# Kernel tuning notes

Hardware: AMD Instinct MI355X
Metric: run time of the kernel (lower is better)

The kernel has to match this reference:

```python
import jax, jax.numpy as jnp
import numpy as np

LN_EPS = 1e-5


def _ln(x, g, b):
    m = x.mean(-1, keepdims=True)
    v = ((x - m) ** 2).mean(-1, keepdims=True)
    return (x - m) * jax.lax.rsqrt(v + LN_EPS) * g + b


def setup_inputs() -> dict:
    key = jax.random.key(0)
    ks = jax.random.split(key, 8)
    B, S, T, Ds, Dt, H = 2, 1024, 1024, 128, 64, 64

    def w(k, shp):
        return jax.random.normal(k, shp, dtype=jnp.float32) * 0.05

    return {
        "source_features": jax.random.normal(ks[0], (B, S, Ds), dtype=jnp.float32),
        "target_features": jax.random.normal(ks[1], (B, T, Dt), dtype=jnp.float32),
        # source_adapter: Linear(Ds,H) -> LN(H) -> ReLU -> Linear(H,H)
        "sW1": w(ks[2], (Ds, H)), "sb1": jnp.zeros(H), "sg": jnp.ones(H), "sbeta": jnp.zeros(H),
        "sW2": w(ks[3], (H, H)), "sb2": jnp.zeros(H),
        # target_adapter: Linear(Dt,H) -> LN(H) -> ReLU -> Linear(H,H)
        "tW1": w(ks[4], (Dt, H)), "tb1": jnp.zeros(H), "tg": jnp.ones(H), "tbeta": jnp.zeros(H),
        "tW2": w(ks[5], (H, H)), "tb2": jnp.zeros(H),
        # city_features: Linear(2H,H) -> LN(H) -> ReLU
        "cW": w(ks[6], (2 * H, H)), "cb": jnp.zeros(H), "cg": jnp.ones(H), "cbeta": jnp.zeros(H),
        # similarity_module: Linear(H,1) -> Sigmoid
        "simW": w(ks[7], (H, 1)), "simb": jnp.zeros(1),
    }


def reference(source_features, target_features,
              sW1, sb1, sg, sbeta, sW2, sb2,
              tW1, tb1, tg, tbeta, tW2, tb2,
              cW, cb, cg, cbeta, simW, simb):
    H = sW2.shape[1]
    s_ad = jax.nn.relu(_ln(source_features @ sW1 + sb1, sg, sbeta)) @ sW2 + sb2  # [B,S,H]
    t_ad = jax.nn.relu(_ln(target_features @ tW1 + tb1, tg, tbeta)) @ tW2 + tb2  # [B,T,H]

    # concat order in torch is [target, source] on the last dim; split the
    # Linear(2H,H) weight so the [B,T,S,2H] concat is never materialized.
    cW_t, cW_s = cW[:H], cW[H:]
    pre = (t_ad @ cW_t)[:, :, None, :] + (s_ad @ cW_s)[:, None, :, :] + cb  # [B,T,S,H]
    h = jax.nn.relu(_ln(pre, cg, cbeta))
    scores = jax.nn.sigmoid((h @ simW)[..., 0] + simb[0])  # [B,T,S]

    attn = jax.nn.softmax(scores, axis=-1)
    transferred = jnp.einsum('bts,bsh->bth', attn, s_ad)
    gate = jax.nn.sigmoid(t_ad.mean(-1, keepdims=True))
    adapted = t_ad * (1.0 - gate) + transferred * gate  # hidden_dim == target_dim: no proj
    return adapted, scores
```

## Files before the change

kernel.cpp:

```cpp
#include <hip/hip_runtime.h>
#include <math.h>

#define BN 2
#define SN 1024
#define TN 1024
#define DS 128
#define DT 64
#define HN 64
#define LN_EPS 1e-5f

typedef float v2f __attribute__((ext_vector_type(2)));

__device__ __forceinline__ float wave_sum(float v) {
#pragma unroll
  for (int m = 32; m >= 1; m >>= 1) v += __shfl_xor(v, m, 64);
  return v;
}

__device__ __forceinline__ v2f lo2(float4 v) { v2f r = {v.x, v.y}; return r; }
__device__ __forceinline__ v2f hi2(float4 v) { v2f r = {v.z, v.w}; return r; }

__global__ __launch_bounds__(256) void k_adapters(
    const float* __restrict__ src, const float* __restrict__ tgt,
    const float* __restrict__ sW1, const float* __restrict__ sb1,
    const float* __restrict__ sg, const float* __restrict__ sbeta,
    const float* __restrict__ sW2, const float* __restrict__ sb2,
    const float* __restrict__ tW1, const float* __restrict__ tb1,
    const float* __restrict__ tg, const float* __restrict__ tbeta,
    const float* __restrict__ tW2, const float* __restrict__ tb2,
    const float* __restrict__ cW, const float* __restrict__ cb,
    float* __restrict__ s_ad, float* __restrict__ sc, float* __restrict__ sstats,
    float* __restrict__ t_ad, float* __restrict__ tc, float* __restrict__ tstats)
{
  __shared__ float xbuf[4][DS];
  __shared__ float rbuf[4][HN];
  int w = threadIdx.x >> 6, lane = threadIdx.x & 63;

  if (blockIdx.x < 512) {
    int row = blockIdx.x * 4 + w;
    xbuf[w][lane]      = src[row * DS + lane];
    xbuf[w][lane + 64] = src[row * DS + 64 + lane];
    float a0 = 0.f, a1 = 0.f, a2_ = 0.f, a3 = 0.f;
#pragma unroll 8
    for (int k = 0; k < DS; k += 4) {
      a0  = fmaf(xbuf[w][k + 0], sW1[(k + 0) * HN + lane], a0);
      a1  = fmaf(xbuf[w][k + 1], sW1[(k + 1) * HN + lane], a1);
      a2_ = fmaf(xbuf[w][k + 2], sW1[(k + 2) * HN + lane], a2_);
      a3  = fmaf(xbuf[w][k + 3], sW1[(k + 3) * HN + lane], a3);
    }
    float h1 = ((a0 + a1) + (a2_ + a3)) + sb1[lane];
    float s1 = wave_sum(h1), s2 = wave_sum(h1 * h1);
    float m = s1 * (1.f / HN);
    float var = s2 * (1.f / HN) - m * m;
    float r = fmaxf(0.f, (h1 - m) * rsqrtf(var + LN_EPS) * sg[lane] + sbeta[lane]);
    rbuf[w][lane] = r;
    float b0 = 0.f, b1 = 0.f, b2 = 0.f, b3 = 0.f;
#pragma unroll 4
    for (int j = 0; j < HN; j += 4) {
      b0 = fmaf(rbuf[w][j + 0], sW2[(j + 0) * HN + lane], b0);
      b1 = fmaf(rbuf[w][j + 1], sW2[(j + 1) * HN + lane], b1);
      b2 = fmaf(rbuf[w][j + 2], sW2[(j + 2) * HN + lane], b2);
      b3 = fmaf(rbuf[w][j + 3], sW2[(j + 3) * HN + lane], b3);
    }
    float a2 = ((b0 + b1) + (b2 + b3)) + sb2[lane];
    s_ad[row * HN + lane] = a2;
    rbuf[w][lane] = a2;
    float c0 = 0.f, c1 = 0.f, c2 = 0.f, c3 = 0.f;
#pragma unroll 4
    for (int j = 0; j < HN; j += 4) {
      c0 = fmaf(rbuf[w][j + 0], cW[(HN + j + 0) * HN + lane], c0);
      c1 = fmaf(rbuf[w][j + 1], cW[(HN + j + 1) * HN + lane], c1);
      c2 = fmaf(rbuf[w][j + 2], cW[(HN + j + 2) * HN + lane], c2);
      c3 = fmaf(rbuf[w][j + 3], cW[(HN + j + 3) * HN + lane], c3);
    }
    float scv = (c0 + c1) + (c2 + c3);
    sc[row * HN + lane] = scv;
    float bs = wave_sum(scv), qs = wave_sum(scv * scv);
    if (lane == 0) { sstats[row * 2] = bs; sstats[row * 2 + 1] = qs; }
  } else {
    int row = (blockIdx.x - 512) * 4 + w;
    xbuf[w][lane] = tgt[row * DT + lane];
    float a0 = 0.f, a1 = 0.f, a2_ = 0.f, a3 = 0.f;
#pragma unroll 4
    for (int k = 0; k < DT; k += 4) {
      a0  = fmaf(xbuf[w][k + 0], tW1[(k + 0) * HN + lane], a0);
      a1  = fmaf(xbuf[w][k + 1], tW1[(k + 1) * HN + lane], a1);
      a2_ = fmaf(xbuf[w][k + 2], tW1[(k + 2) * HN + lane], a2_);
      a3  = fmaf(xbuf[w][k + 3], tW1[(k + 3) * HN + lane], a3);
    }
    float h1 = ((a0 + a1) + (a2_ + a3)) + tb1[lane];
    float s1 = wave_sum(h1), s2 = wave_sum(h1 * h1);
    float m = s1 * (1.f / HN);
    float var = s2 * (1.f / HN) - m * m;
    float r = fmaxf(0.f, (h1 - m) * rsqrtf(var + LN_EPS) * tg[lane] + tbeta[lane]);
    rbuf[w][lane] = r;
    float b0 = 0.f, b1 = 0.f, b2 = 0.f, b3 = 0.f;
#pragma unroll 4
    for (int j = 0; j < HN; j += 4) {
      b0 = fmaf(rbuf[w][j + 0], tW2[(j + 0) * HN + lane], b0);
      b1 = fmaf(rbuf[w][j + 1], tW2[(j + 1) * HN + lane], b1);
      b2 = fmaf(rbuf[w][j + 2], tW2[(j + 2) * HN + lane], b2);
      b3 = fmaf(rbuf[w][j + 3], tW2[(j + 3) * HN + lane], b3);
    }
    float a2 = ((b0 + b1) + (b2 + b3)) + tb2[lane];
    t_ad[row * HN + lane] = a2;
    float asum = wave_sum(a2);
    float gate = 1.f / (1.f + __expf(-asum * (1.f / HN)));
    rbuf[w][lane] = a2;
    float c0 = 0.f, c1 = 0.f, c2 = 0.f, c3 = 0.f;
#pragma unroll 4
    for (int j = 0; j < HN; j += 4) {
      c0 = fmaf(rbuf[w][j + 0], cW[(j + 0) * HN + lane], c0);
      c1 = fmaf(rbuf[w][j + 1], cW[(j + 1) * HN + lane], c1);
      c2 = fmaf(rbuf[w][j + 2], cW[(j + 2) * HN + lane], c2);
      c3 = fmaf(rbuf[w][j + 3], cW[(j + 3) * HN + lane], c3);
    }
    float tcv = ((c0 + c1) + (c2 + c3)) + cb[lane];
    tc[row * HN + lane] = tcv;
    float A = wave_sum(tcv), Q = wave_sum(tcv * tcv);
    if (lane == 0) { tstats[row * 3] = A; tstats[row * 3 + 1] = Q; tstats[row * 3 + 2] = gate; }
  }
}

#define ROWDW 68
#define CHUNKDW (64 * ROWDW)

__global__ __attribute__((amdgpu_flat_work_group_size(512, 512)))
__attribute__((amdgpu_waves_per_eu(4, 4)))
void k_scores(
    const float* __restrict__ cg, const float* __restrict__ cbeta,
    const float* __restrict__ simW, const float* __restrict__ simb,
    const float* __restrict__ sc, const float* __restrict__ sstats,
    const float* __restrict__ tc, const float* __restrict__ tstats,
    float* __restrict__ out_scores)
{
  __shared__ float tile[2 * CHUNKDW];
  int tid = threadIdx.x;
  int w = tid >> 6, lane = tid & 63;
  int sblk = blockIdx.x & 3;
  int tblk = (blockIdx.x >> 2) & 63;
  int b    = blockIdx.x >> 8;
  int t0 = tblk * 16 + w * 2;
  int rt0 = __builtin_amdgcn_readfirstlane(b * TN + t0);
  int rt1 = rt0 + 1;

  float A0  = tstats[rt0 * 3 + 0];
  float Qt0 = tstats[rt0 * 3 + 1];
  float A1  = tstats[rt1 * 3 + 0];
  float Qt1 = tstats[rt1 * 3 + 1];
  const float4* tq0 = (const float4*)(tc + rt0 * HN);
  const float4* tq1 = (const float4*)(tc + rt1 * HN);
  const float4* cgq = (const float4*)cg;
  const float4* cbq = (const float4*)cbeta;
  const float4* swq = (const float4*)simW;
  float simb0 = simb[0];

  const float4* scg = (const float4*)(sc + b * SN * HN);
  int s0 = sblk * 256;

  int r0s = tid >> 4, gs = tid & 15;
  int d0 = r0s * ROWDW + gs * 4;
  int d1 = d0 + 32 * ROWDW;

  {
    float4 v0 = scg[(s0 + r0s) * 16 + gs];
    float4 v1 = scg[(s0 + r0s + 32) * 16 + gs];
    *(float4*)&tile[d0] = v0;
    *(float4*)&tile[d1] = v1;
  }
  __syncthreads();

  const v2f zero2 = {0.f, 0.f};

#pragma unroll 1
  for (int c = 0; c < 4; ++c) {
    float4 p0, p1;
    if (c < 3) {
      int sn = s0 + (c + 1) * 64;
      p0 = scg[(sn + r0s) * 16 + gs];
      p1 = scg[(sn + r0s + 32) * 16 + gs];
    }

    const float* tb_ = &tile[(c & 1) * CHUNKDW + lane * ROWDW];
    int s = s0 + c * 64 + lane;
    float2 bq = *(const float2*)&sstats[(b * SN + s) * 2];

    float4 q0, q1, q2, q3, q4, q5, q6, q7, q8, q9, q10, q11, q12, q13, q14, q15;
#define LOADQ(i) q##i = *(const float4*)&tb_[(i) * 4]
    LOADQ(0); LOADQ(1); LOADQ(2); LOADQ(3); LOADQ(4); LOADQ(5); LOADQ(6); LOADQ(7);
    LOADQ(8); LOADQ(9); LOADQ(10); LOADQ(11); LOADQ(12); LOADQ(13); LOADQ(14); LOADQ(15);
#undef LOADQ

    v2f D0a = zero2, D0b = zero2, D1a = zero2, D1b = zero2;
#define P1(i) do { \
      float4 ta = tq0[i]; float4 tbv = tq1[i]; \
      D0a = __builtin_elementwise_fma(lo2(ta),  lo2(q##i), D0a); \
      D0b = __builtin_elementwise_fma(hi2(ta),  hi2(q##i), D0b); \
      D1a = __builtin_elementwise_fma(lo2(tbv), lo2(q##i), D1a); \
      D1b = __builtin_elementwise_fma(hi2(tbv), hi2(q##i), D1b); \
    } while (0)
    P1(0); P1(1); P1(2); P1(3); P1(4); P1(5); P1(6); P1(7);
    P1(8); P1(9); P1(10); P1(11); P1(12); P1(13); P1(14); P1(15);
#undef P1
    v2f Ds0 = D0a + D0b, Ds1 = D1a + D1b;
    float D_0 = Ds0.x + Ds0.y;
    float D_1 = Ds1.x + Ds1.y;

    float mean0  = (A0 + bq.x) * (1.f / HN);
    float var0   = (Qt0 + bq.y + 2.f * D_0) * (1.f / HN) - mean0 * mean0;
    float alpha0 = rsqrtf(var0 + LN_EPS);
    float mean1  = (A1 + bq.x) * (1.f / HN);
    float var1   = (Qt1 + bq.y + 2.f * D_1) * (1.f / HN) - mean1 * mean1;
    float alpha1 = rsqrtf(var1 + LN_EPS);

    v2f m0 = {mean0, mean0}, a0v = {alpha0, alpha0};
    v2f m1 = {mean1, mean1}, a1v = {alpha1, alpha1};
    v2f dt0a = zero2, dt0b = zero2, dt1a = zero2, dt1b = zero2;

#define P2(i) do { \
      float4 c4 = cgq[i]; float4 b4 = cbq[i]; float4 w4 = swq[i]; \
      float4 ta = tq0[i]; float4 tbv = tq1[i]; \
      { v2f u = lo2(q##i) + lo2(ta);  v2f z = u - m0; v2f P = a0v * lo2(c4); \
        v2f n = __builtin_elementwise_fma(z, P, lo2(b4)); \
        v2f r = __builtin_elementwise_max(n, zero2); \
        dt0a = __builtin_elementwise_fma(r, lo2(w4), dt0a); } \
      { v2f u = hi2(q##i) + hi2(ta);  v2f z = u - m0; v2f P = a0v * hi2(c4); \
        v2f n = __builtin_elementwise_fma(z, P, hi2(b4)); \
        v2f r = __builtin_elementwise_max(n, zero2); \
        dt0b = __builtin_elementwise_fma(r, hi2(w4), dt0b); } \
      { v2f u = lo2(q##i) + lo2(tbv); v2f z = u - m1; v2f P = a1v * lo2(c4); \
        v2f n = __builtin_elementwise_fma(z, P, lo2(b4)); \
        v2f r = __builtin_elementwise_max(n, zero2); \
        dt1a = __builtin_elementwise_fma(r, lo2(w4), dt1a); } \
      { v2f u = hi2(q##i) + hi2(tbv); v2f z = u - m1; v2f P = a1v * hi2(c4); \
        v2f n = __builtin_elementwise_fma(z, P, hi2(b4)); \
        v2f r = __builtin_elementwise_max(n, zero2); \
        dt1b = __builtin_elementwise_fma(r, hi2(w4), dt1b); } \
    } while (0)
    P2(0); P2(1); P2(2); P2(3); P2(4); P2(5); P2(6); P2(7);
    P2(8); P2(9); P2(10); P2(11); P2(12); P2(13); P2(14); P2(15);
#undef P2
    v2f dd0 = dt0a + dt0b, dd1 = dt1a + dt1b;
    float dot0 = dd0.x + dd0.y;
    float dot1 = dd1.x + dd1.y;
    float score0 = 1.f / (1.f + __expf(-(dot0 + simb0)));
    float score1 = 1.f / (1.f + __expf(-(dot1 + simb0)));
    out_scores[rt0 * SN + s] = score0;
    out_scores[rt1 * SN + s] = score1;

    if (c < 3) {
      int dst = ((c + 1) & 1) * CHUNKDW;
      *(float4*)&tile[dst + d0] = p0;
      *(float4*)&tile[dst + d1] = p1;
    }
    __syncthreads();
  }
}

__global__ __launch_bounds__(256, 4) void k_xfer(
    const float* __restrict__ scores, const float* __restrict__ s_ad,
    float* __restrict__ xpart, float* __restrict__ epart)
{
  __shared__ float eLDS[4][16][64];
  __shared__ float part[4][16][64];
  __shared__ float esum[4][16];
  int tid = threadIdx.x;
  int w = __builtin_amdgcn_readfirstlane(tid >> 6);
  int lane = tid & 63;
  int sblk = blockIdx.x & 3;
  int tblk = (blockIdx.x >> 2) & 63;
  int b    = blockIdx.x >> 8;
  int t0 = tblk * 16;
  int soff = sblk * 256 + w * 64;

#pragma unroll 4
  for (int t = 0; t < 16; ++t) {
    int rt = __builtin_amdgcn_readfirstlane(b * TN + t0 + t);
    float ev = __expf(scores[rt * SN + soff + lane]);
    eLDS[w][t][lane] = ev;
    float es = wave_sum(ev);
    if (lane == 0) esum[w][t] = es;
  }

  const float* sadb = s_ad + b * SN * HN;
  float acc[16];
#pragma unroll
  for (int t = 0; t < 16; ++t) acc[t] = 0.f;
#pragma unroll 4
  for (int si4 = 0; si4 < 16; ++si4) {
    int sbase = soff + si4 * 4;
    float sv0 = sadb[(sbase + 0) * HN + lane];
    float sv1 = sadb[(sbase + 1) * HN + lane];
    float sv2 = sadb[(sbase + 2) * HN + lane];
    float sv3 = sadb[(sbase + 3) * HN + lane];
#pragma unroll
    for (int t = 0; t < 16; ++t) {
      float4 e4 = *(const float4*)&eLDS[w][t][si4 * 4];
      acc[t] = fmaf(e4.x, sv0, acc[t]);
      acc[t] = fmaf(e4.y, sv1, acc[t]);
      acc[t] = fmaf(e4.z, sv2, acc[t]);
      acc[t] = fmaf(e4.w, sv3, acc[t]);
    }
  }

#pragma unroll
  for (int t = 0; t < 16; ++t) part[w][t][lane] = acc[t];
  __syncthreads();
#pragma unroll
  for (int k = 0; k < 4; ++k) {
    int c2 = tid + k * 256;
    int t = c2 >> 6, h = c2 & 63;
    float sum = part[0][t][h] + part[1][t][h] + part[2][t][h] + part[3][t][h];
    int rt = b * TN + t0 + t;
    xpart[(rt * 4 + sblk) * HN + h] = sum;
  }
  if (tid < 16) {
    float es = esum[0][tid] + esum[1][tid] + esum[2][tid] + esum[3][tid];
    int rt = b * TN + t0 + tid;
    epart[rt * 4 + sblk] = es;
  }
}

__global__ __launch_bounds__(256) void k_final(
    const float* __restrict__ xpart, const float* __restrict__ epart,
    const float* __restrict__ t_ad, const float* __restrict__ tstats,
    float* __restrict__ out_adapted)
{
  int tid = threadIdx.x;
  int tl = tid >> 6, h = tid & 63;
  int rt = blockIdx.x * 4 + tl;
  float x = xpart[(rt * 4 + 0) * HN + h] + xpart[(rt * 4 + 1) * HN + h]
          + xpart[(rt * 4 + 2) * HN + h] + xpart[(rt * 4 + 3) * HN + h];
  float es = epart[rt * 4 + 0] + epart[rt * 4 + 1]
           + epart[rt * 4 + 2] + epart[rt * 4 + 3];
  float tr = x / es;
  float gate = tstats[rt * 3 + 2];
  float tad = t_ad[rt * HN + h];
  out_adapted[rt * HN + h] = tad * (1.f - gate) + tr * gate;
}

extern "C" void kernel_launch(void* const* d_in, const int* in_sizes, int n_in,
                              void* d_out, int out_size, void* d_ws, size_t ws_size,
                              hipStream_t stream) {
  const float* src   = (const float*)d_in[0];
  const float* tgt   = (const float*)d_in[1];
  const float* sW1   = (const float*)d_in[2];
  const float* sb1   = (const float*)d_in[3];
  const float* sg    = (const float*)d_in[4];
  const float* sbeta = (const float*)d_in[5];
  const float* sW2   = (const float*)d_in[6];
  const float* sb2   = (const float*)d_in[7];
  const float* tW1   = (const float*)d_in[8];
  const float* tb1   = (const float*)d_in[9];
  const float* tg    = (const float*)d_in[10];
  const float* tbeta = (const float*)d_in[11];
  const float* tW2   = (const float*)d_in[12];
  const float* tb2   = (const float*)d_in[13];
  const float* cW    = (const float*)d_in[14];
  const float* cb    = (const float*)d_in[15];
  const float* cg    = (const float*)d_in[16];
  const float* cbeta = (const float*)d_in[17];
  const float* simW  = (const float*)d_in[18];
  const float* simb  = (const float*)d_in[19];

  float* ws     = (float*)d_ws;
  float* s_ad   = ws;
  float* sc     = ws + 131072;
  float* sstats = ws + 262144;
  float* t_ad   = ws + 266240;
  float* tc     = ws + 397312;
  float* tstats = ws + 528384;
  float* xpart  = ws + 534528;
  float* epart  = ws + 1058816;

  float* out_adapted = (float*)d_out;
  float* out_scores  = (float*)d_out + 131072;

  hipLaunchKernelGGL(k_adapters, dim3(1024), dim3(256), 0, stream,
                     src, tgt, sW1, sb1, sg, sbeta, sW2, sb2,
                     tW1, tb1, tg, tbeta, tW2, tb2, cW, cb,
                     s_ad, sc, sstats, t_ad, tc, tstats);
  hipLaunchKernelGGL(k_scores, dim3(BN * 64 * 4), dim3(512), 0, stream,
                     cg, cbeta, simW, simb, sc, sstats, tc, tstats, out_scores);
  hipLaunchKernelGGL(k_xfer, dim3(BN * 64 * 4), dim3(256), 0, stream,
                     out_scores, s_ad, xpart, epart);
  hipLaunchKernelGGL(k_final, dim3(512), dim3(256), 0, stream,
                     xpart, epart, t_ad, tstats, out_adapted);
}
```

Baseline: 169.4 us.

## Split k_scores into one 64-source chunk per block, dropping double-buffered loop

The scores kernel no longer loops over four 64-row source chunks with an LDS double buffer and prefetch. Each block now handles a single chunk, and the grid grows fourfold (2048 blocks). The waves_per_eu pin is replaced by plain launch_bounds, and the source tile is reread from LDS in both passes instead of being held in registers. The aim is more parallelism and less register pressure, at the cost of reloading the t-row stats and tc vectors four times as often and paying more block launch overhead.

```diff
diff --git a/kernel.cpp b/kernel.cpp
--- a/kernel.cpp
+++ b/kernel.cpp
@@ -123,26 +123,23 @@
 }
 
 #define ROWDW 68
-#define CHUNKDW (64 * ROWDW)
-
-__global__ __attribute__((amdgpu_flat_work_group_size(512, 512)))
-__attribute__((amdgpu_waves_per_eu(4, 4)))
-void k_scores(
+__global__ __launch_bounds__(512) void k_scores(
     const float* __restrict__ cg, const float* __restrict__ cbeta,
     const float* __restrict__ simW, const float* __restrict__ simb,
     const float* __restrict__ sc, const float* __restrict__ sstats,
     const float* __restrict__ tc, const float* __restrict__ tstats,
     float* __restrict__ out_scores)
 {
-  __shared__ float tile[2 * CHUNKDW];
+  __shared__ float tile[64 * ROWDW];
   int tid = threadIdx.x;
   int w = tid >> 6, lane = tid & 63;
-  int sblk = blockIdx.x & 3;
-  int tblk = (blockIdx.x >> 2) & 63;
-  int b    = blockIdx.x >> 8;
+  int sblk = blockIdx.x & 15;
+  int tblk = (blockIdx.x >> 4) & 63;
+  int b    = blockIdx.x >> 10;
   int t0 = tblk * 16 + w * 2;
   int rt0 = __builtin_amdgcn_readfirstlane(b * TN + t0);
   int rt1 = rt0 + 1;
+  int s0 = sblk * 64;
 
   float A0  = tstats[rt0 * 3 + 0];
   float Qt0 = tstats[rt0 * 3 + 1];
@@ -156,105 +153,75 @@
   float simb0 = simb[0];
 
   const float4* scg = (const float4*)(sc + b * SN * HN);
-  int s0 = sblk * 256;
-
-  int r0s = tid >> 4, gs = tid & 15;
-  int d0 = r0s * ROWDW + gs * 4;
-  int d1 = d0 + 32 * ROWDW;
 
   {
+    int r0s = tid >> 4, gs = tid & 15;
     float4 v0 = scg[(s0 + r0s) * 16 + gs];
     float4 v1 = scg[(s0 + r0s + 32) * 16 + gs];
-    *(float4*)&tile[d0] = v0;
-    *(float4*)&tile[d1] = v1;
+    *(float4*)&tile[r0s * ROWDW + gs * 4] = v0;
+    *(float4*)&tile[(r0s + 32) * ROWDW + gs * 4] = v1;
   }
   __syncthreads();
 
   const v2f zero2 = {0.f, 0.f};
-
-#pragma unroll 1
-  for (int c = 0; c < 4; ++c) {
-    float4 p0, p1;
-    if (c < 3) {
-      int sn = s0 + (c + 1) * 64;
-      p0 = scg[(sn + r0s) * 16 + gs];
-      p1 = scg[(sn + r0s + 32) * 16 + gs];
-    }
-
-    const float* tb_ = &tile[(c & 1) * CHUNKDW + lane * ROWDW];
-    int s = s0 + c * 64 + lane;
-    float2 bq = *(const float2*)&sstats[(b * SN + s) * 2];
-
-    float4 q0, q1, q2, q3, q4, q5, q6, q7, q8, q9, q10, q11, q12, q13, q14, q15;
-#define LOADQ(i) q##i = *(const float4*)&tb_[(i) * 4]
-    LOADQ(0); LOADQ(1); LOADQ(2); LOADQ(3); LOADQ(4); LOADQ(5); LOADQ(6); LOADQ(7);
-    LOADQ(8); LOADQ(9); LOADQ(10); LOADQ(11); LOADQ(12); LOADQ(13); LOADQ(14); LOADQ(15);
-#undef LOADQ
-
-    v2f D0a = zero2, D0b = zero2, D1a = zero2, D1b = zero2;
-#define P1(i) do { \
-      float4 ta = tq0[i]; float4 tbv = tq1[i]; \
-      D0a = __builtin_elementwise_fma(lo2(ta),  lo2(q##i), D0a); \
-      D0b = __builtin_elementwise_fma(hi2(ta),  hi2(q##i), D0b); \
-      D1a = __builtin_elementwise_fma(lo2(tbv), lo2(q##i), D1a); \
-      D1b = __builtin_elementwise_fma(hi2(tbv), hi2(q##i), D1b); \
-    } while (0)
-    P1(0); P1(1); P1(2); P1(3); P1(4); P1(5); P1(6); P1(7);
-    P1(8); P1(9); P1(10); P1(11); P1(12); P1(13); P1(14); P1(15);
-#undef P1
-    v2f Ds0 = D0a + D0b, Ds1 = D1a + D1b;
-    float D_0 = Ds0.x + Ds0.y;
-    float D_1 = Ds1.x + Ds1.y;
-
-    float mean0  = (A0 + bq.x) * (1.f / HN);
-    float var0   = (Qt0 + bq.y + 2.f * D_0) * (1.f / HN) - mean0 * mean0;
-    float alpha0 = rsqrtf(var0 + LN_EPS);
-    float mean1  = (A1 + bq.x) * (1.f / HN);
-    float var1   = (Qt1 + bq.y + 2.f * D_1) * (1.f / HN) - mean1 * mean1;
-    float alpha1 = rsqrtf(var1 + LN_EPS);
-
-    v2f m0 = {mean0, mean0}, a0v = {alpha0, alpha0};
-    v2f m1 = {mean1, mean1}, a1v = {alpha1, alpha1};
-    v2f dt0a = zero2, dt0b = zero2, dt1a = zero2, dt1b = zero2;
-
-#define P2(i) do { \
-      float4 c4 = cgq[i]; float4 b4 = cbq[i]; float4 w4 = swq[i]; \
-      float4 ta = tq0[i]; float4 tbv = tq1[i]; \
-      { v2f u = lo2(q##i) + lo2(ta);  v2f z = u - m0; v2f P = a0v * lo2(c4); \
-        v2f n = __builtin_elementwise_fma(z, P, lo2(b4)); \
-        v2f r = __builtin_elementwise_max(n, zero2); \
-        dt0a = __builtin_elementwise_fma(r, lo2(w4), dt0a); } \
-      { v2f u = hi2(q##i) + hi2(ta);  v2f z = u - m0; v2f P = a0v * hi2(c4); \
-        v2f n = __builtin_elementwise_fma(z, P, hi2(b4)); \
-        v2f r = __builtin_elementwise_max(n, zero2); \
-        dt0b = __builtin_elementwise_fma(r, hi2(w4), dt0b); } \
-      { v2f u = lo2(q##i) + lo2(tbv); v2f z = u - m1; v2f P = a1v * lo2(c4); \
-        v2f n = __builtin_elementwise_fma(z, P, lo2(b4)); \
-        v2f r = __builtin_elementwise_max(n, zero2); \
-        dt1a = __builtin_elementwise_fma(r, lo2(w4), dt1a); } \
-      { v2f u = hi2(q##i) + hi2(tbv); v2f z = u - m1; v2f P = a1v * hi2(c4); \
-        v2f n = __builtin_elementwise_fma(z, P, hi2(b4)); \
-        v2f r = __builtin_elementwise_max(n, zero2); \
-        dt1b = __builtin_elementwise_fma(r, hi2(w4), dt1b); } \
-    } while (0)
-    P2(0); P2(1); P2(2); P2(3); P2(4); P2(5); P2(6); P2(7);
-    P2(8); P2(9); P2(10); P2(11); P2(12); P2(13); P2(14); P2(15);
-#undef P2
-    v2f dd0 = dt0a + dt0b, dd1 = dt1a + dt1b;
-    float dot0 = dd0.x + dd0.y;
-    float dot1 = dd1.x + dd1.y;
-    float score0 = 1.f / (1.f + __expf(-(dot0 + simb0)));
-    float score1 = 1.f / (1.f + __expf(-(dot1 + simb0)));
-    out_scores[rt0 * SN + s] = score0;
-    out_scores[rt1 * SN + s] = score1;
-
-    if (c < 3) {
-      int dst = ((c + 1) & 1) * CHUNKDW;
-      *(float4*)&tile[dst + d0] = p0;
-      *(float4*)&tile[dst + d1] = p1;
-    }
-    __syncthreads();
-  }
+  const float* tb_ = &tile[lane * ROWDW];
+  int s = s0 + lane;
+  float2 bq = *(const float2*)&sstats[(b * SN + s) * 2];
+
+  v2f D0a = zero2, D0b = zero2, D1a = zero2, D1b = zero2;
+#pragma unroll
+  for (int g = 0; g < 16; ++g) {
+    float4 v = *(const float4*)&tb_[g * 4];
+    float4 ta = tq0[g]; float4 tbv = tq1[g];
+    D0a = __builtin_elementwise_fma(lo2(ta),  lo2(v), D0a);
+    D0b = __builtin_elementwise_fma(hi2(ta),  hi2(v), D0b);
+    D1a = __builtin_elementwise_fma(lo2(tbv), lo2(v), D1a);
+    D1b = __builtin_elementwise_fma(hi2(tbv), hi2(v), D1b);
+  }
+  v2f Ds0 = D0a + D0b, Ds1 = D1a + D1b;
+  float D_0 = Ds0.x + Ds0.y;
+  float D_1 = Ds1.x + Ds1.y;
+
+  float mean0  = (A0 + bq.x) * (1.f / HN);
+  float var0   = (Qt0 + bq.y + 2.f * D_0) * (1.f / HN) - mean0 * mean0;
+  float alpha0 = rsqrtf(var0 + LN_EPS);
+  float mean1  = (A1 + bq.x) * (1.f / HN);
+  float var1   = (Qt1 + bq.y + 2.f * D_1) * (1.f / HN) - mean1 * mean1;
+  float alpha1 = rsqrtf(var1 + LN_EPS);
+
+  v2f m0 = {mean0, mean0}, a0v = {alpha0, alpha0};
+  v2f m1 = {mean1, mean1}, a1v = {alpha1, alpha1};
+  v2f dt0a = zero2, dt0b = zero2, dt1a = zero2, dt1b = zero2;
+
+#pragma unroll
+  for (int g = 0; g < 16; ++g) {
+    float4 v  = *(const float4*)&tb_[g * 4];
+    float4 c4 = cgq[g]; float4 b4 = cbq[g]; float4 w4 = swq[g];
+    float4 ta = tq0[g]; float4 tbv = tq1[g];
+    { v2f u = lo2(v) + lo2(ta);  v2f z = u - m0; v2f P = a0v * lo2(c4);
+      v2f n = __builtin_elementwise_fma(z, P, lo2(b4));
+      v2f r = __builtin_elementwise_max(n, zero2);
+      dt0a = __builtin_elementwise_fma(r, lo2(w4), dt0a); }
+    { v2f u = hi2(v) + hi2(ta);  v2f z = u - m0; v2f P = a0v * hi2(c4);
+      v2f n = __builtin_elementwise_fma(z, P, hi2(b4));
+      v2f r = __builtin_elementwise_max(n, zero2);
+      dt0b = __builtin_elementwise_fma(r, hi2(w4), dt0b); }
+    { v2f u = lo2(v) + lo2(tbv); v2f z = u - m1; v2f P = a1v * lo2(c4);
+      v2f n = __builtin_elementwise_fma(z, P, lo2(b4));
+      v2f r = __builtin_elementwise_max(n, zero2);
+      dt1a = __builtin_elementwise_fma(r, lo2(w4), dt1a); }
+    { v2f u = hi2(v) + hi2(tbv); v2f z = u - m1; v2f P = a1v * hi2(c4);
+      v2f n = __builtin_elementwise_fma(z, P, hi2(b4));
+      v2f r = __builtin_elementwise_max(n, zero2);
+      dt1b = __builtin_elementwise_fma(r, hi2(w4), dt1b); }
+  }
+  v2f dd0 = dt0a + dt0b, dd1 = dt1a + dt1b;
+  float dot0 = dd0.x + dd0.y;
+  float dot1 = dd1.x + dd1.y;
+  float score0 = 1.f / (1.f + __expf(-(dot0 + simb0)));
+  float score1 = 1.f / (1.f + __expf(-(dot1 + simb0)));
+  out_scores[rt0 * SN + s] = score0;
+  out_scores[rt1 * SN + s] = score1;
 }
 
 __global__ __launch_bounds__(256, 4) void k_xfer(
@@ -380,7 +347,7 @@
                      src, tgt, sW1, sb1, sg, sbeta, sW2, sb2,
                      tW1, tb1, tg, tbeta, tW2, tb2, cW, cb,
                      s_ad, sc, sstats, t_ad, tc, tstats);
-  hipLaunchKernelGGL(k_scores, dim3(BN * 64 * 4), dim3(512), 0, stream,
+  hipLaunchKernelGGL(k_scores, dim3(BN * 64 * 16), dim3(512), 0, stream,
                      cg, cbeta, simW, simb, sc, sstats, tc, tstats, out_scores);
   hipLaunchKernelGGL(k_xfer, dim3(BN * 64 * 4), dim3(256), 0, stream,
                      out_scores, s_ad, xpart, epart);
```

After: 151.9 us (median of 2 runs). 10.4% less time.
